# Kernel tuning notes

Hardware: AMD Instinct MI355X
Metric: run time of the kernel (lower is better)

## Reference

```python
import jax, jax.numpy as jnp
import numpy as np
from jax import lax

SEQ_LEN = 1024
INPUT_DIM = 64
NUM_HIDDEN = 512
NUM_CLASSES = 10
BATCH = 256
SIGMA = 0.01


def setup_inputs() -> dict:
    key = jax.random.key(0)
    k_x, k_whx, k_whh, k_wph = jax.random.split(key, 4)
    x = jax.random.normal(k_x, (BATCH, SEQ_LEN, INPUT_DIM), dtype=jnp.float32)
    Whx = SIGMA * jax.random.normal(k_whx, (INPUT_DIM, NUM_HIDDEN), dtype=jnp.float32)
    Whh = SIGMA * jax.random.normal(k_whh, (NUM_HIDDEN, NUM_HIDDEN), dtype=jnp.float32)
    Wph = SIGMA * jax.random.normal(k_wph, (NUM_HIDDEN, NUM_CLASSES), dtype=jnp.float32)
    bh = jnp.zeros((NUM_HIDDEN, 1), dtype=jnp.float32)
    bp = jnp.zeros((NUM_CLASSES, 1), dtype=jnp.float32)
    return {"x": x, "Whx": Whx, "Whh": Whh, "Wph": Wph, "bh": bh, "bp": bp}


def reference(x, Whx, Whh, Wph, bh, bp):
    # x: [B, S, D]; h: [B, H]
    B = x.shape[0]
    H = Whh.shape[0]
    bh_row = bh[:, 0]  # per-hidden-unit bias (intended semantics of bh)
    bp_row = bp[:, 0]

    def step(h, xt):
        h_new = jnp.tanh(xt @ Whx + h @ Whh + bh_row)
        return h_new, None

    h0 = jnp.zeros((B, H), dtype=x.dtype)
    xs = jnp.swapaxes(x, 0, 1)  # [S, B, D] for scan over time
    h_final, _ = lax.scan(step, h0, xs)
    p = h_final @ Wph + bp_row  # [B, C]
    return p
```

## Files before the change

### kernel.cpp

```cpp
#include <hip/hip_runtime.h>
#include <hip/hip_bf16.h>
#include <hip/hip_fp8.h>
#include <cstdint>
#include <cstddef>


#define T_SEQ   1024
#define D_IN    64
#define H_DIM   512
#define NB      16
#define NBLK    16
#define NTW     4
#define KS_F16  10
#define KS_REG8 2
#define KS_LDS8 4
#define HSPLIT  320
#define APITCH  848
#define FP8OFF  640
#define ABUF_BYTES (2 * NB * APITCH)
#define WWAVE_BYTES (KS_LDS8 * 2 * 1024)
#define WLDS_BYTES (8 * WWAVE_BYTES)
#define SMEM_TOTAL (ABUF_BYTES + WLDS_BYTES)
#define WSCALE  256.0f
#define HSCALE  128.0f
#define UNSCALE (1.0f / 32768.0f)
#define U_BYTES ((size_t)T_SEQ * NBLK * 512 * 32)
#define TTP     64

typedef __attribute__((ext_vector_type(8))) short  short8;
typedef __attribute__((ext_vector_type(4))) short  short4v;
typedef __attribute__((ext_vector_type(4))) float  f32x4;
typedef __attribute__((ext_vector_type(4))) unsigned int uint4v;
typedef __attribute__((ext_vector_type(2))) unsigned int uint2v;

static __device__ __forceinline__ short f16b(float v) {
  return __builtin_bit_cast(short, (_Float16)v);
}
static __device__ __forceinline__ short bf16b(float v) {
  return __builtin_bit_cast(short, __float2bfloat16(v));
}
static __device__ __forceinline__ float f16f(unsigned short u) {
  return (float)__builtin_bit_cast(_Float16, (short)u);
}
static __device__ __forceinline__ unsigned int pk2h(float a, float b) {
#if defined(__has_builtin) && __has_builtin(__builtin_amdgcn_cvt_pkrtz)
  return __builtin_bit_cast(unsigned int, __builtin_amdgcn_cvt_pkrtz(a, b));
#else
  return (unsigned int)(unsigned short)f16b(a) |
         ((unsigned int)(unsigned short)f16b(b) << 16);
#endif
}
static __device__ __forceinline__ float fast_tanh(float x) {
  const float t = __builtin_amdgcn_exp2f(x * 2.885390081777927f);
  return 1.f - 2.f * __builtin_amdgcn_rcpf(t + 1.f);
}
static __device__ __forceinline__ unsigned char f32_to_fp8(float v) {
#if defined(__has_builtin) && __has_builtin(__builtin_amdgcn_cvt_pk_fp8_f32)
  const int r = __builtin_amdgcn_cvt_pk_fp8_f32(v, v, 0, false);
  return (unsigned char)(r & 0xff);
#else
  __hip_fp8_e4m3 f(v);
  return (unsigned char)f.__x;
#endif
}
static __device__ __forceinline__ unsigned int pk4fp8(float a, float b, float c, float d) {
#if defined(__has_builtin) && __has_builtin(__builtin_amdgcn_cvt_pk_fp8_f32)
  int r = __builtin_amdgcn_cvt_pk_fp8_f32(a, b, 0, false);
  r = __builtin_amdgcn_cvt_pk_fp8_f32(c, d, r, true);
  return (unsigned int)r;
#else
  return (unsigned int)f32_to_fp8(a) | ((unsigned int)f32_to_fp8(b) << 8) |
         ((unsigned int)f32_to_fp8(c) << 16) | ((unsigned int)f32_to_fp8(d) << 24);
#endif
}
static __device__ __forceinline__ float fp8_to_f32(unsigned char b) {
  __hip_fp8_e4m3 f;
  f.__x = (__hip_fp8_storage_t)b;
  return (float)f;
}

__global__ __launch_bounds__(512, 2)
void rnn_u_precompute(const float* __restrict__ x, const float* __restrict__ Whx,
                      const float* __restrict__ bh, char* __restrict__ U)
{
  const int tid  = threadIdx.x;
  const int lane = tid & 63;
  const int w    = tid >> 6;
  const int n16  = lane & 15;
  const int kq   = lane >> 4;
  const int wg   = blockIdx.x;
  const int cwave = w * 64;

  short8 wa[2][NTW];
  #pragma unroll
  for (int s = 0; s < 2; ++s) {
    #pragma unroll
    for (int nt = 0; nt < NTW; ++nt) {
      const int c = cwave + nt * 16 + n16;
      short8 f;
      #pragma unroll
      for (int j = 0; j < 8; ++j)
        f[j] = f16b(Whx[(size_t)(s * 32 + kq * 8 + j) * H_DIM + c]);
      wa[s][nt] = f;
    }
  }
  f32x4 bb[NTW];
  #pragma unroll
  for (int nt = 0; nt < NTW; ++nt) {
    #pragma unroll
    for (int i = 0; i < 4; ++i) bb[nt][i] = bh[cwave + nt * 16 + kq * 4 + i];
  }

  const int b = wg * NB + n16;
  const float* pxb = x + (size_t)b * T_SEQ * D_IN + kq * 8;
  const int t0 = blockIdx.y * TTP;

  f32x4 c0, c1, c2, c3;
  {
    const float* p = pxb + (size_t)t0 * D_IN;
    c0 = *(const f32x4*)p;        c1 = *(const f32x4*)(p + 4);
    c2 = *(const f32x4*)(p + 32); c3 = *(const f32x4*)(p + 36);
  }

  for (int tt = 0; tt < TTP; ++tt) {
    const int t = t0 + tt;
    f32x4 n0, n1, n2, n3;
    if (tt + 1 < TTP) {
      const float* p = pxb + (size_t)(t + 1) * D_IN;
      n0 = *(const f32x4*)p;        n1 = *(const f32x4*)(p + 4);
      n2 = *(const f32x4*)(p + 32); n3 = *(const f32x4*)(p + 36);
    }
    short8 xb0, xb1;
    xb0[0]=f16b(c0.x); xb0[1]=f16b(c0.y); xb0[2]=f16b(c0.z); xb0[3]=f16b(c0.w);
    xb0[4]=f16b(c1.x); xb0[5]=f16b(c1.y); xb0[6]=f16b(c1.z); xb0[7]=f16b(c1.w);
    xb1[0]=f16b(c2.x); xb1[1]=f16b(c2.y); xb1[2]=f16b(c2.z); xb1[3]=f16b(c2.w);
    xb1[4]=f16b(c3.x); xb1[5]=f16b(c3.y); xb1[6]=f16b(c3.z); xb1[7]=f16b(c3.w);

    f32x4 D[NTW];
    #pragma unroll
    for (int nt = 0; nt < NTW; ++nt) {
      D[nt] = bb[nt];
      D[nt] = __builtin_amdgcn_mfma_f32_16x16x32_f16(wa[0][nt], xb0, D[nt], 0, 0, 0);
      D[nt] = __builtin_amdgcn_mfma_f32_16x16x32_f16(wa[1][nt], xb1, D[nt], 0, 0, 0);
    }
    uint4v o0, o1;
    o0.x = pk2h(D[0][0], D[0][1]); o0.y = pk2h(D[0][2], D[0][3]);
    o0.z = pk2h(D[1][0], D[1][1]); o0.w = pk2h(D[1][2], D[1][3]);
    o1.x = pk2h(D[2][0], D[2][1]); o1.y = pk2h(D[2][2], D[2][3]);
    o1.z = pk2h(D[3][0], D[3][1]); o1.w = pk2h(D[3][2], D[3][3]);
    char* dst = U + (((size_t)t * NBLK + wg) * 512 + tid) * 32;
    *(uint4v*)dst = o0;
    *(uint4v*)(dst + 16) = o1;

    c0 = n0; c1 = n1; c2 = n2; c3 = n3;
  }
}

__global__ __launch_bounds__(512, 2)
void VanillaRNN_70025146794452_kernel(
    const float* __restrict__ Whh,
    const float* __restrict__ Wph,
    const float* __restrict__ bp,
    const char* __restrict__ U,
    float* __restrict__ out)
{
  const int tid  = threadIdx.x;
  const int lane = tid & 63;
  const int w    = tid >> 6;
  const int n16  = lane & 15;
  const int kq   = lane >> 4;
  const int rbase = blockIdx.x * NB;
  const int cwave = w * 64;

  extern __shared__ char smem[];
  char* Ab  = smem;
  char* Wlw = smem + ABUF_BYTES + w * WWAVE_BYTES;

  short8 wr[KS_F16][NTW];
  #pragma unroll
  for (int s = 0; s < KS_F16; ++s) {
    #pragma unroll
    for (int nt = 0; nt < NTW; ++nt) {
      const int c = cwave + nt * 16 + n16;
      short8 f;
      #pragma unroll
      for (int j = 0; j < 8; ++j)
        f[j] = f16b(Whh[(size_t)(s * 32 + kq * 8 + j) * H_DIM + c]);
      wr[s][nt] = f;
    }
  }
  long long wf8[KS_REG8][NTW];
  #pragma unroll
  for (int s = 0; s < KS_REG8; ++s) {
    #pragma unroll
    for (int nt = 0; nt < NTW; ++nt) {
      const int c  = cwave + nt * 16 + n16;
      const int k0 = (KS_F16 + s) * 32 + kq * 8;
      unsigned int lo = 0, hi = 0;
      #pragma unroll
      for (int bi = 0; bi < 4; ++bi) {
        lo |= ((unsigned int)f32_to_fp8(Whh[(size_t)(k0 + bi) * H_DIM + c] * WSCALE)) << (8 * bi);
        hi |= ((unsigned int)f32_to_fp8(Whh[(size_t)(k0 + 4 + bi) * H_DIM + c] * WSCALE)) << (8 * bi);
      }
      wf8[s][nt] = (long long)(((unsigned long long)hi << 32) | lo);
    }
  }
  for (int sl = 0; sl < KS_LDS8; ++sl) {
    for (int half = 0; half < 2; ++half) {
      const int k0 = (KS_F16 + KS_REG8 + sl) * 32 + kq * 8;
      unsigned int bqq[4];
      #pragma unroll
      for (int hh = 0; hh < 2; ++hh) {
        const int c = cwave + (2 * half + hh) * 16 + n16;
        #pragma unroll
        for (int u = 0; u < 2; ++u) {
          unsigned int acc = 0;
          #pragma unroll
          for (int bi = 0; bi < 4; ++bi)
            acc |= ((unsigned int)f32_to_fp8(Whh[(size_t)(k0 + u * 4 + bi) * H_DIM + c] * WSCALE)) << (8 * bi);
          bqq[hh * 2 + u] = acc;
        }
      }
      uint4v pk; pk.x = bqq[0]; pk.y = bqq[1]; pk.z = bqq[2]; pk.w = bqq[3];
      *(uint4v*)(Wlw + (size_t)(sl * 2 + half) * 1024 + lane * 16) = pk;
    }
  }

  for (int i = tid; i < ABUF_BYTES / 4; i += 512) ((int*)Ab)[i] = 0;
  uint4v Upf0, Upf1;
  {
    const char* up = U + (((size_t)0 * NBLK + blockIdx.x) * 512 + tid) * 32;
    Upf0 = *(const uint4v*)up;
    Upf1 = *(const uint4v*)(up + 16);
  }

  f32x4 C[NTW], C2[NTW];

  for (int t = 0; t < T_SEQ; ++t) {
    __syncthreads();
    char* Ac = Ab + (t & 1) * (NB * APITCH);
    char* An = Ab + ((t + 1) & 1) * (NB * APITCH);

    short8 hb = *(const short8*)(Ac + n16 * APITCH + 0 * 64 + kq * 16);

    C[0][0]=f16f(Upf0.x&0xffff); C[0][1]=f16f(Upf0.x>>16);
    C[0][2]=f16f(Upf0.y&0xffff); C[0][3]=f16f(Upf0.y>>16);
    C[1][0]=f16f(Upf0.z&0xffff); C[1][1]=f16f(Upf0.z>>16);
    C[1][2]=f16f(Upf0.w&0xffff); C[1][3]=f16f(Upf0.w>>16);
    C[2][0]=f16f(Upf1.x&0xffff); C[2][1]=f16f(Upf1.x>>16);
    C[2][2]=f16f(Upf1.y&0xffff); C[2][3]=f16f(Upf1.y>>16);
    C[3][0]=f16f(Upf1.z&0xffff); C[3][1]=f16f(Upf1.z>>16);
    C[3][2]=f16f(Upf1.w&0xffff); C[3][3]=f16f(Upf1.w>>16);
    #pragma unroll
    for (int nt = 0; nt < NTW; ++nt) C2[nt] = (f32x4){0.f, 0.f, 0.f, 0.f};

    {
      const int t1 = (t + 1 < T_SEQ) ? (t + 1) : (T_SEQ - 1);
      const char* up = U + (((size_t)t1 * NBLK + blockIdx.x) * 512 + tid) * 32;
      Upf0 = *(const uint4v*)up;
      Upf1 = *(const uint4v*)(up + 16);
    }

    #pragma unroll
    for (int s = 0; s < KS_F16; ++s) {
      const short8 a = hb;
      if (s + 1 < KS_F16)
        hb = *(const short8*)(Ac + n16 * APITCH + (s + 1) * 64 + kq * 16);
      #pragma unroll
      for (int nt = 0; nt < NTW; ++nt)
        C[nt] = __builtin_amdgcn_mfma_f32_16x16x32_f16(wr[s][nt], a, C[nt], 0, 0, 0);
    }
    #pragma unroll
    for (int s = 0; s < KS_REG8; ++s) {
      const long long h8 = *(const long long*)(Ac + n16 * APITCH + FP8OFF + s * 32 + kq * 8);
      #pragma unroll
      for (int nt = 0; nt < NTW; ++nt)
        C2[nt] = __builtin_amdgcn_mfma_f32_16x16x32_fp8_fp8(wf8[s][nt], h8, C2[nt], 0, 0, 0);
    }
    #pragma unroll
    for (int sl = 0; sl < KS_LDS8; ++sl) {
      const long long h8 = *(const long long*)(Ac + n16 * APITCH + FP8OFF + (KS_REG8 + sl) * 32 + kq * 8);
      const uint4v q0 = *(const uint4v*)(Wlw + (size_t)(sl * 2 + 0) * 1024 + lane * 16);
      const uint4v q1 = *(const uint4v*)(Wlw + (size_t)(sl * 2 + 1) * 1024 + lane * 16);
      const long long w0 = (long long)(((unsigned long long)q0.y << 32) | q0.x);
      const long long w1 = (long long)(((unsigned long long)q0.w << 32) | q0.z);
      const long long w2 = (long long)(((unsigned long long)q1.y << 32) | q1.x);
      const long long w3 = (long long)(((unsigned long long)q1.w << 32) | q1.z);
      C2[0] = __builtin_amdgcn_mfma_f32_16x16x32_fp8_fp8(w0, h8, C2[0], 0, 0, 0);
      C2[1] = __builtin_amdgcn_mfma_f32_16x16x32_fp8_fp8(w1, h8, C2[1], 0, 0, 0);
      C2[2] = __builtin_amdgcn_mfma_f32_16x16x32_fp8_fp8(w2, h8, C2[2], 0, 0, 0);
      C2[3] = __builtin_amdgcn_mfma_f32_16x16x32_fp8_fp8(w3, h8, C2[3], 0, 0, 0);
    }

    char* drow = An + n16 * APITCH;
    if (cwave < HSPLIT) {
      #pragma unroll
      for (int nt = 0; nt < NTW; ++nt) {
        const int c0 = cwave + nt * 16 + kq * 4;
        float v0 = fast_tanh(fmaf(C2[nt][0], UNSCALE, C[nt][0]));
        float v1 = fast_tanh(fmaf(C2[nt][1], UNSCALE, C[nt][1]));
        float v2 = fast_tanh(fmaf(C2[nt][2], UNSCALE, C[nt][2]));
        float v3 = fast_tanh(fmaf(C2[nt][3], UNSCALE, C[nt][3]));
        uint2v o; o.x = pk2h(v0, v1); o.y = pk2h(v2, v3);
        *(uint2v*)(drow + c0 * 2) = o;
      }
    } else {
      #pragma unroll
      for (int nt = 0; nt < NTW; ++nt) {
        const int c0 = cwave + nt * 16 + kq * 4;
        float v0 = fast_tanh(fmaf(C2[nt][0], UNSCALE, C[nt][0]));
        float v1 = fast_tanh(fmaf(C2[nt][1], UNSCALE, C[nt][1]));
        float v2 = fast_tanh(fmaf(C2[nt][2], UNSCALE, C[nt][2]));
        float v3 = fast_tanh(fmaf(C2[nt][3], UNSCALE, C[nt][3]));
        *(unsigned int*)(drow + FP8OFF + (c0 - HSPLIT)) =
            pk4fp8(v0 * HSCALE, v1 * HSCALE, v2 * HSCALE, v3 * HSCALE);
      }
    }
  }

  __syncthreads();
  if (tid < NB * 10) {
    const int r = tid / 10, c = tid % 10;
    const char* row = Ab + r * APITCH;
    float acc = bp[c];
    #pragma unroll 8
    for (int k = 0; k < HSPLIT; ++k)
      acc += f16f(*(const unsigned short*)(row + k * 2)) * Wph[k * 10 + c];
    #pragma unroll 8
    for (int k = HSPLIT; k < H_DIM; ++k)
      acc += fp8_to_f32((unsigned char)row[FP8OFF + (k - HSPLIT)]) * (1.f / HSCALE) * Wph[k * 10 + c];
    out[(size_t)(rbase + r) * 10 + c] = acc;
  }
}

#define FB_APITCH  1040
#define FB_FP8OFF  768
#define FB_ABUF    (2 * NB * FB_APITCH)
#define FB_WWAVE   (6 * 2 * 1024)
#define FB_SMEM    (FB_ABUF + 8 * FB_WWAVE)

__global__ __launch_bounds__(512, 2)
void rnn_fallback_kernel(
    const float* __restrict__ x, const float* __restrict__ Whx,
    const float* __restrict__ Whh, const float* __restrict__ Wph,
    const float* __restrict__ bh, const float* __restrict__ bp,
    float* __restrict__ out)
{
  const int tid = threadIdx.x, lane = tid & 63, w = tid >> 6;
  const int n16 = lane & 15, kq = lane >> 4;
  const int rbase = blockIdx.x * NB, cwave = w * 64;
  extern __shared__ char smem[];
  char* Ab  = smem;
  char* Wlw = smem + FB_ABUF + w * FB_WWAVE;

  short8 wr[12 * 4];
  #pragma unroll
  for (int s = 0; s < 12; ++s)
    #pragma unroll
    for (int nt = 0; nt < 4; ++nt) {
      const int c = cwave + nt * 16 + n16, k0 = s * 32 + kq * 8;
      short8 f;
      #pragma unroll
      for (int j = 0; j < 8; ++j) {
        const int k = k0 + j;
        const float* src = (k < D_IN) ? (Whx + (size_t)k * H_DIM + c)
                                      : (Whh + (size_t)(k - D_IN) * H_DIM + c);
        f[j] = bf16b(*src);
      }
      wr[s * 4 + nt] = f;
    }
  for (int s = 0; s < 6; ++s)
    for (int pp = 0; pp < 2; ++pp) {
      const int k0 = (12 + s) * 32 + kq * 8;
      unsigned int bq[4];
      #pragma unroll
      for (int half = 0; half < 2; ++half) {
        const int c = cwave + (2 * pp + half) * 16 + n16;
        #pragma unroll
        for (int u = 0; u < 2; ++u) {
          unsigned int acc = 0;
          #pragma unroll
          for (int bi = 0; bi < 4; ++bi)
            acc |= ((unsigned int)f32_to_fp8(Whh[(size_t)(k0 + u * 4 + bi - D_IN) * H_DIM + c] * WSCALE)) << (8 * bi);
          bq[half * 2 + u] = acc;
        }
      }
      uint4v pk; pk.x = bq[0]; pk.y = bq[1]; pk.z = bq[2]; pk.w = bq[3];
      *(uint4v*)(Wlw + (size_t)(s * 2 + pp) * 1024 + lane * 16) = pk;
    }
  float bhreg[4];
  #pragma unroll
  for (int nt = 0; nt < 4; ++nt) bhreg[nt] = bh[cwave + nt * 16 + n16];
  for (int i = tid; i < FB_ABUF / 4; i += 512) ((int*)Ab)[i] = 0;
  const int xr = (tid >> 4) & 15, xc4 = (tid & 15) * 4;
  if (tid < 256) {
    const f32x4 xv = *(const f32x4*)(x + ((size_t)(rbase + xr) * T_SEQ) * D_IN + xc4);
    short4v s4; s4[0]=bf16b(xv.x); s4[1]=bf16b(xv.y); s4[2]=bf16b(xv.z); s4[3]=bf16b(xv.w);
    *(short4v*)(Ab + xr * FB_APITCH + xc4 * 2) = s4;
  }
  f32x4 C[4], C2[4];
  for (int t = 0; t < T_SEQ; ++t) {
    __syncthreads();
    char* Ac = Ab + (t & 1) * (NB * FB_APITCH);
    char* An = Ab + ((t + 1) & 1) * (NB * FB_APITCH);
    const int t1 = (t + 1 < T_SEQ) ? (t + 1) : (T_SEQ - 1);
    f32x4 xv;
    if (tid < 256)
      xv = *(const f32x4*)(x + ((size_t)(rbase + xr) * T_SEQ + t1) * D_IN + xc4);
    #pragma unroll
    for (int nt = 0; nt < 4; ++nt) {
      C[nt] = (f32x4){0.f,0.f,0.f,0.f}; C2[nt] = (f32x4){0.f,0.f,0.f,0.f};
    }
    #pragma unroll
    for (int s = 0; s < 12; ++s) {
      const short8 a = *(const short8*)(Ac + n16 * FB_APITCH + s * 64 + kq * 16);
      #pragma unroll
      for (int nt = 0; nt < 4; ++nt)
        C[nt] = __builtin_amdgcn_mfma_f32_16x16x32_bf16(a, wr[s * 4 + nt], C[nt], 0, 0, 0);
    }
    #pragma unroll
    for (int s = 0; s < 6; ++s) {
      const long long a8 = *(const long long*)(Ac + n16 * FB_APITCH + FB_FP8OFF + s * 32 + kq * 8);
      #pragma unroll
      for (int pp = 0; pp < 2; ++pp) {
        const uint4v q = *(const uint4v*)(Wlw + (size_t)(s * 2 + pp) * 1024 + lane * 16);
        const long long b0 = (long long)(((unsigned long long)q.y << 32) | q.x);
        const long long b1 = (long long)(((unsigned long long)q.w << 32) | q.z);
        C2[2*pp]   = __builtin_amdgcn_mfma_f32_16x16x32_fp8_fp8(a8, b0, C2[2*pp],   0, 0, 0);
        C2[2*pp+1] = __builtin_amdgcn_mfma_f32_16x16x32_fp8_fp8(a8, b1, C2[2*pp+1], 0, 0, 0);
      }
    }
    if (tid < 256) {
      short4v s4; s4[0]=bf16b(xv.x); s4[1]=bf16b(xv.y); s4[2]=bf16b(xv.z); s4[3]=bf16b(xv.w);
      *(short4v*)(An + xr * FB_APITCH + xc4 * 2) = s4;
    }
    const int row0 = kq * 4;
    #pragma unroll
    for (int nt = 0; nt < 4; ++nt) {
      const int cbase = cwave + nt * 16;
      #pragma unroll
      for (int i = 0; i < 4; ++i) {
        const float v = fast_tanh(fmaf(C2[nt][i], UNSCALE, C[nt][i]) + bhreg[nt]);
        char* dst = An + (row0 + i) * FB_APITCH;
        if (cbase < 320) *(short*)(dst + 128 + (cbase + n16) * 2) = bf16b(v);
        else dst[FB_FP8OFF + (cbase + n16 - 320)] = f32_to_fp8(v * HSCALE);
      }
    }
  }
  __syncthreads();
  if (tid < NB * 10) {
    const int r = tid / 10, c = tid % 10;
    const char* row = Ab + r * FB_APITCH;
    float acc = bp[c];
    #pragma unroll 8
    for (int k = 0; k < 320; ++k) {
      const __hip_bfloat16 hb = __builtin_bit_cast(__hip_bfloat16, *(const short*)(row + 128 + k * 2));
      acc += __bfloat162float(hb) * Wph[k * 10 + c];
    }
    #pragma unroll 8
    for (int k = 320; k < H_DIM; ++k)
      acc += fp8_to_f32((unsigned char)row[FB_FP8OFF + (k - 320)]) * (1.f / HSCALE) * Wph[k * 10 + c];
    out[(size_t)(rbase + r) * 10 + c] = acc;
  }
}

extern "C" void kernel_launch(void* const* d_in, const int* in_sizes, int n_in,
                              void* d_out, int out_size, void* d_ws, size_t ws_size,
                              hipStream_t stream) {
  const float* x   = (const float*)d_in[0];
  const float* Whx = (const float*)d_in[1];
  const float* Whh = (const float*)d_in[2];
  const float* Wph = (const float*)d_in[3];
  const float* bh  = (const float*)d_in[4];
  const float* bp  = (const float*)d_in[5];
  float* out = (float*)d_out;

  if (ws_size >= U_BYTES) {
    char* U = (char*)d_ws;
    (void)hipFuncSetAttribute((const void*)VanillaRNN_70025146794452_kernel,
                              hipFuncAttributeMaxDynamicSharedMemorySize, SMEM_TOTAL);
    rnn_u_precompute<<<dim3(NBLK, T_SEQ / TTP), dim3(512), 0, stream>>>(x, Whx, bh, U);
    VanillaRNN_70025146794452_kernel<<<dim3(NBLK), dim3(512), SMEM_TOTAL, stream>>>(
        Whh, Wph, bp, U, out);
  } else {
    (void)hipFuncSetAttribute((const void*)rnn_fallback_kernel,
                              hipFuncAttributeMaxDynamicSharedMemorySize, FB_SMEM);
    rnn_fallback_kernel<<<dim3(NBLK), dim3(512), FB_SMEM, stream>>>(
        x, Whx, Whh, Wph, bh, bp, out);
  }
}
```

Baseline: 1.848 ms.

## Use MX-scaled 16x16x128 FP8 MFMA and keep all FP8 weights in registers

Replaces four of the six 16x16x32 FP8 MFMA k-steps per tile with a single scaled 16x16x128 f8f6f4 MFMA, using a unit scale of 0x7F. The FP8 weights for those rows now sit in 8-int registers, so the per-wave LDS weight staging and its per-step LDS reads go away. This cuts MFMA instruction count and LDS traffic on the serial recurrence's critical path, but raises register pressure and depends on the builtin existing, falling back to six register-resident FP8 steps otherwise. The wider MFMA uses a different K lane mapping, so the weight and h packing must match it for results to stay correct.

Result: no change. 1.841 ms (-0.3%).

```diff
diff --git a/kernel.cpp b/kernel.cpp
--- a/kernel.cpp
+++ b/kernel.cpp
@@ -12,15 +12,12 @@
 #define NBLK    16
 #define NTW     4
 #define KS_F16  10
-#define KS_REG8 2
-#define KS_LDS8 4
+#define KS_TL8  2
 #define HSPLIT  320
 #define APITCH  848
 #define FP8OFF  640
 #define ABUF_BYTES (2 * NB * APITCH)
-#define WWAVE_BYTES (KS_LDS8 * 2 * 1024)
-#define WLDS_BYTES (8 * WWAVE_BYTES)
-#define SMEM_TOTAL (ABUF_BYTES + WLDS_BYTES)
+#define SMEM_TOTAL ABUF_BYTES
 #define WSCALE  256.0f
 #define HSCALE  128.0f
 #define UNSCALE (1.0f / 32768.0f)
@@ -32,6 +29,16 @@
 typedef __attribute__((ext_vector_type(4))) float  f32x4;
 typedef __attribute__((ext_vector_type(4))) unsigned int uint4v;
 typedef __attribute__((ext_vector_type(2))) unsigned int uint2v;
+typedef __attribute__((ext_vector_type(8))) int    int8v;
+
+#if defined(__has_builtin)
+#if __has_builtin(__builtin_amdgcn_mfma_scale_f32_16x16x128_f8f6f4)
+#define HAVE_MX 1
+#endif
+#endif
+#ifndef HAVE_MX
+#define HAVE_MX 0
+#endif
 
 static __device__ __forceinline__ short f16b(float v) {
   return __builtin_bit_cast(short, (_Float16)v);
@@ -173,8 +180,7 @@
   const int cwave = w * 64;
 
   extern __shared__ char smem[];
-  char* Ab  = smem;
-  char* Wlw = smem + ABUF_BYTES + w * WWAVE_BYTES;
+  char* Ab = smem;
 
   short8 wr[KS_F16][NTW];
   #pragma unroll
@@ -189,42 +195,59 @@
       wr[s][nt] = f;
     }
   }
-  long long wf8[KS_REG8][NTW];
-  #pragma unroll
-  for (int s = 0; s < KS_REG8; ++s) {
+
+#if HAVE_MX
+  int8v wmx[NTW];
+  #pragma unroll
+  for (int nt = 0; nt < NTW; ++nt) {
+    const int c = cwave + nt * 16 + n16;
+    int8v v;
+    #pragma unroll
+    for (int d = 0; d < 8; ++d) {
+      unsigned acc = 0;
+      #pragma unroll
+      for (int bi = 0; bi < 4; ++bi) {
+        const int k = HSPLIT + kq * 32 + d * 4 + bi;
+        acc |= ((unsigned)f32_to_fp8(Whh[(size_t)k * H_DIM + c] * WSCALE)) << (8 * bi);
+      }
+      v[d] = (int)acc;
+    }
+    wmx[nt] = v;
+  }
+  long long wt8[KS_TL8][NTW];
+  #pragma unroll
+  for (int s = 0; s < KS_TL8; ++s) {
     #pragma unroll
     for (int nt = 0; nt < NTW; ++nt) {
       const int c  = cwave + nt * 16 + n16;
-      const int k0 = (KS_F16 + s) * 32 + kq * 8;
-      unsigned int lo = 0, hi = 0;
+      const int k0 = HSPLIT + 128 + s * 32 + kq * 8;
+      unsigned lo = 0, hi = 0;
       #pragma unroll
       for (int bi = 0; bi < 4; ++bi) {
-        lo |= ((unsigned int)f32_to_fp8(Whh[(size_t)(k0 + bi) * H_DIM + c] * WSCALE)) << (8 * bi);
-        hi |= ((unsigned int)f32_to_fp8(Whh[(size_t)(k0 + 4 + bi) * H_DIM + c] * WSCALE)) << (8 * bi);
-      }
-      wf8[s][nt] = (long long)(((unsigned long long)hi << 32) | lo);
-    }
-  }
-  for (int sl = 0; sl < KS_LDS8; ++sl) {
-    for (int half = 0; half < 2; ++half) {
-      const int k0 = (KS_F16 + KS_REG8 + sl) * 32 + kq * 8;
-      unsigned int bqq[4];
-      #pragma unroll
-      for (int hh = 0; hh < 2; ++hh) {
-        const int c = cwave + (2 * half + hh) * 16 + n16;
-        #pragma unroll
-        for (int u = 0; u < 2; ++u) {
-          unsigned int acc = 0;
-          #pragma unroll
-          for (int bi = 0; bi < 4; ++bi)
-            acc |= ((unsigned int)f32_to_fp8(Whh[(size_t)(k0 + u * 4 + bi) * H_DIM + c] * WSCALE)) << (8 * bi);
-          bqq[hh * 2 + u] = acc;
-        }
-      }
-      uint4v pk; pk.x = bqq[0]; pk.y = bqq[1]; pk.z = bqq[2]; pk.w = bqq[3];
-      *(uint4v*)(Wlw + (size_t)(sl * 2 + half) * 1024 + lane * 16) = pk;
-    }
-  }
+        lo |= ((unsigned)f32_to_fp8(Whh[(size_t)(k0 + bi) * H_DIM + c] * WSCALE)) << (8 * bi);
+        hi |= ((unsigned)f32_to_fp8(Whh[(size_t)(k0 + 4 + bi) * H_DIM + c] * WSCALE)) << (8 * bi);
+      }
+      wt8[s][nt] = (long long)(((unsigned long long)hi << 32) | lo);
+    }
+  }
+#else
+  long long wt8[6][NTW];
+  #pragma unroll
+  for (int s = 0; s < 6; ++s) {
+    #pragma unroll
+    for (int nt = 0; nt < NTW; ++nt) {
+      const int c  = cwave + nt * 16 + n16;
+      const int k0 = HSPLIT + s * 32 + kq * 8;
+      unsigned lo = 0, hi = 0;
+      #pragma unroll
+      for (int bi = 0; bi < 4; ++bi) {
+        lo |= ((unsigned)f32_to_fp8(Whh[(size_t)(k0 + bi) * H_DIM + c] * WSCALE)) << (8 * bi);
+        hi |= ((unsigned)f32_to_fp8(Whh[(size_t)(k0 + 4 + bi) * H_DIM + c] * WSCALE)) << (8 * bi);
+      }
+      wt8[s][nt] = (long long)(((unsigned long long)hi << 32) | lo);
+    }
+  }
+#endif
 
   for (int i = tid; i < ABUF_BYTES / 4; i += 512) ((int*)Ab)[i] = 0;
   uint4v Upf0, Upf1;
@@ -270,27 +293,36 @@
       for (int nt = 0; nt < NTW; ++nt)
         C[nt] = __builtin_amdgcn_mfma_f32_16x16x32_f16(wr[s][nt], a, C[nt], 0, 0, 0);
     }
-    #pragma unroll
-    for (int s = 0; s < KS_REG8; ++s) {
+
+#if HAVE_MX
+    {
+      const char* hp = Ac + n16 * APITCH + FP8OFF + kq * 32;
+      const uint4v m0 = *(const uint4v*)hp;
+      const uint4v m1 = *(const uint4v*)(hp + 16);
+      int8v hmx;
+      hmx[0]=(int)m0.x; hmx[1]=(int)m0.y; hmx[2]=(int)m0.z; hmx[3]=(int)m0.w;
+      hmx[4]=(int)m1.x; hmx[5]=(int)m1.y; hmx[6]=(int)m1.z; hmx[7]=(int)m1.w;
+      #pragma unroll
+      for (int nt = 0; nt < NTW; ++nt)
+        C2[nt] = __builtin_amdgcn_mfma_scale_f32_16x16x128_f8f6f4(
+            wmx[nt], hmx, C2[nt], 0, 0, 0, 0x7F7F7F7F, 0, 0x7F7F7F7F);
+    }
+    #pragma unroll
+    for (int s = 0; s < KS_TL8; ++s) {
+      const long long h8 = *(const long long*)(Ac + n16 * APITCH + FP8OFF + 128 + s * 32 + kq * 8);
+      #pragma unroll
+      for (int nt = 0; nt < NTW; ++nt)
+        C2[nt] = __builtin_amdgcn_mfma_f32_16x16x32_fp8_fp8(wt8[s][nt], h8, C2[nt], 0, 0, 0);
+    }
+#else
+    #pragma unroll
+    for (int s = 0; s < 6; ++s) {
       const long long h8 = *(const long long*)(Ac + n16 * APITCH + FP8OFF + s * 32 + kq * 8);
       #pragma unroll
       for (int nt = 0; nt < NTW; ++nt)
-        C2[nt] = __builtin_amdgcn_mfma_f32_16x16x32_fp8_fp8(wf8[s][nt], h8, C2[nt], 0, 0, 0);
-    }
-    #pragma unroll
-    for (int sl = 0; sl < KS_LDS8; ++sl) {
-      const long long h8 = *(const long long*)(Ac + n16 * APITCH + FP8OFF + (KS_REG8 + sl) * 32 + kq * 8);
-      const uint4v q0 = *(const uint4v*)(Wlw + (size_t)(sl * 2 + 0) * 1024 + lane * 16);
-      const uint4v q1 = *(const uint4v*)(Wlw + (size_t)(sl * 2 + 1) * 1024 + lane * 16);
-      const long long w0 = (long long)(((unsigned long long)q0.y << 32) | q0.x);
-      const long long w1 = (long long)(((unsigned long long)q0.w << 32) | q0.z);
-      const long long w2 = (long long)(((unsigned long long)q1.y << 32) | q1.x);
-      const long long w3 = (long long)(((unsigned long long)q1.w << 32) | q1.z);
-      C2[0] = __builtin_amdgcn_mfma_f32_16x16x32_fp8_fp8(w0, h8, C2[0], 0, 0, 0);
-      C2[1] = __builtin_amdgcn_mfma_f32_16x16x32_fp8_fp8(w1, h8, C2[1], 0, 0, 0);
-      C2[2] = __builtin_amdgcn_mfma_f32_16x16x32_fp8_fp8(w2, h8, C2[2], 0, 0, 0);
-      C2[3] = __builtin_amdgcn_mfma_f32_16x16x32_fp8_fp8(w3, h8, C2[3], 0, 0, 0);
-    }
+        C2[nt] = __builtin_amdgcn_mfma_f32_16x16x32_fp8_fp8(wt8[s][nt], h8, C2[nt], 0, 0, 0);
+    }
+#endif
 
     char* drow = An + n16 * APITCH;
     if (cwave < HSPLIT) {
```
